# Optimization experiments

Hardware: AMD Instinct MI355X
Metric: run time of the kernel (lower is better)

## Reference

```python
import jax, jax.numpy as jnp
import numpy as np

# Static config matching init_kwargs / input_specs
B, C, H, W, T = 2, 128, 32, 32, 32
OUT = 256
WS, SHIFT, HEADS = 4, 2, 8
MLP = 4 * C
N = WS ** 3          # tokens per 4x4x4 window = 64
D_BLOCKS = 4         # depth=2 -> 2 (no-shift, shift) pairs


def _rel_idx():
    coords = np.stack(np.meshgrid(np.arange(WS), np.arange(WS), np.arange(WS), indexing='ij')).reshape(3, -1)
    rel = (coords[:, :, None] - coords[:, None, :]).transpose(1, 2, 0) + (WS - 1)
    return (rel[..., 0] * (2 * WS - 1) ** 2 + rel[..., 1] * (2 * WS - 1) + rel[..., 2]).astype(np.int32)

REL_IDX = jnp.asarray(_rel_idx())  # [N, N]


def _attn_mask():
    # Faithful port of Block.createmask (H,W,T already multiples of WS)
    img = np.zeros((H, W, T))
    sl = (slice(0, -WS), slice(-WS, -SHIFT), slice(-SHIFT, None))
    cnt = 0
    for hs in sl:
        for ws_ in sl:
            for ts in sl:
                img[hs, ws_, ts] = cnt
                cnt += 1
    m = img.reshape(H // WS, WS, W // WS, WS, T // WS, WS).transpose(0, 2, 4, 1, 3, 5).reshape(-1, N)
    am = m[:, None, :] - m[:, :, None]
    return jnp.asarray(np.where(am != 0, -100.0, 0.0).astype(np.float32))  # [nW, N, N]

MASK = _attn_mask()


def _partition(x):  # [b,H,W,T,c] -> [b*nW, N, c]
    b, c = x.shape[0], x.shape[-1]
    x = x.reshape(b, H // WS, WS, W // WS, WS, T // WS, WS, c).transpose(0, 1, 3, 5, 2, 4, 6, 7)
    return x.reshape(-1, N, c)


def _reverse(wins, b, c):  # [b*nW, N, c] -> [b,H,W,T,c]
    x = wins.reshape(b, H // WS, W // WS, T // WS, WS, WS, WS, c).transpose(0, 1, 4, 2, 5, 3, 6, 7)
    return x.reshape(b, H, W, T, c)


def _ln(x, g, b):
    mu = x.mean(-1, keepdims=True)
    var = ((x - mu) ** 2).mean(-1, keepdims=True)
    return (x - mu) / jnp.sqrt(var + 1e-5) * g + b


def _swin(x, shift, g1, b1, qw, qb, pw, pb, rpb, g2, b2, f1w, f1b, f2w, f2b):
    b, L, c = x.shape
    hd = c // HEADS
    scale = hd ** -0.5
    h = _ln(x, g1, b1).reshape(b, H, W, T, c)
    if shift:
        h = jnp.roll(h, (-SHIFT, -SHIFT, -SHIFT), axis=(1, 2, 3))
    win = _partition(h)  # [b*nW, N, c]
    qkv = (win @ qw.T + qb).reshape(-1, N, 3, HEADS, hd).transpose(2, 0, 3, 1, 4)
    q, k, v = qkv[0] * scale, qkv[1], qkv[2]
    attn = jnp.einsum('bhnd,bhmd->bhnm', q, k) + rpb[REL_IDX].transpose(2, 0, 1)[None]
    if shift:
        nW = MASK.shape[0]
        attn = (attn.reshape(b, nW, HEADS, N, N) + MASK[None, :, None]).reshape(-1, HEADS, N, N)
    attn = jax.nn.softmax(attn, axis=-1)
    o = jnp.einsum('bhnm,bhmd->bhnd', attn, v).transpose(0, 2, 1, 3).reshape(-1, N, c)
    o = o @ pw.T + pb
    h = _reverse(o, b, c)
    if shift:
        h = jnp.roll(h, (SHIFT, SHIFT, SHIFT), axis=(1, 2, 3))
    x = x + h.reshape(b, L, c)
    m = jax.nn.gelu(_ln(x, g2, b2) @ f1w.T + f1b, approximate=False)
    return x + (m @ f2w.T + f2b)


def setup_inputs() -> dict:
    key = jax.random.key(0)
    ks = jax.random.split(key, 10)
    r = lambda i, sh, s=0.02: jax.random.normal(ks[i], sh, jnp.float32) * s
    Dn = D_BLOCKS
    return {
        'x': jax.random.normal(ks[0], (B, C, H, W, T), jnp.float32),
        'norm1_g': jnp.ones((Dn, C), jnp.float32), 'norm1_b': jnp.zeros((Dn, C), jnp.float32),
        'qkv_w': r(1, (Dn, 3 * C, C)), 'qkv_b': jnp.zeros((Dn, 3 * C), jnp.float32),
        'proj_w': r(2, (Dn, C, C)), 'proj_b': jnp.zeros((Dn, C), jnp.float32),
        'rpb': r(3, (Dn, (2 * WS - 1) ** 3, HEADS)),
        'norm2_g': jnp.ones((Dn, C), jnp.float32), 'norm2_b': jnp.zeros((Dn, C), jnp.float32),
        'fc1_w': r(4, (Dn, MLP, C)), 'fc1_b': jnp.zeros((Dn, MLP), jnp.float32),
        'fc2_w': r(5, (Dn, C, MLP)), 'fc2_b': jnp.zeros((Dn, C), jnp.float32),
        'dw_w': r(6, (C, 1, 3, 3, 3), 0.1), 'dw_b': jnp.zeros((C,), jnp.float32),
        'pw_w': r(7, (OUT, C, 1, 1, 1), 0.05), 'pw_b': jnp.zeros((OUT,), jnp.float32),
        'bn_g': jnp.ones((OUT,), jnp.float32), 'bn_b': jnp.zeros((OUT,), jnp.float32),
    }


def reference(x, norm1_g, norm1_b, qkv_w, qkv_b, proj_w, proj_b, rpb, norm2_g, norm2_b,
              fc1_w, fc1_b, fc2_w, fc2_b, dw_w, dw_b, pw_w, pw_b, bn_g, bn_b):
    b = x.shape[0]
    t = x.transpose(0, 2, 3, 4, 1).reshape(b, H * W * T, C)  # b (h w t) c
    shifts = [0, SHIFT, 0, SHIFT]
    for i, s in enumerate(shifts):
        t = _swin(t, s, norm1_g[i], norm1_b[i], qkv_w[i], qkv_b[i], proj_w[i], proj_b[i],
                  rpb[i], norm2_g[i], norm2_b[i], fc1_w[i], fc1_b[i], fc2_w[i], fc2_b[i])
    y = t.reshape(b, H, W, T, C).transpose(0, 4, 1, 2, 3)
    # connectBlock: depthwise 3x3x3 conv + pointwise 1x1x1 conv + BatchNorm3d + ReLU
    dn = ('NCDHW', 'OIDHW', 'NCDHW')
    y = jax.lax.conv_general_dilated(y, dw_w, (1, 1, 1), 'SAME', dimension_numbers=dn,
                                     feature_group_count=C) + dw_b[None, :, None, None, None]
    y = jax.lax.conv_general_dilated(y, pw_w, (1, 1, 1), 'SAME', dimension_numbers=dn) + pw_b[None, :, None, None, None]
    mu = y.mean((0, 2, 3, 4), keepdims=True)
    var = ((y - mu) ** 2).mean((0, 2, 3, 4), keepdims=True)
    y = (y - mu) / jnp.sqrt(var + 1e-5) * bn_g[None, :, None, None, None] + bn_b[None, :, None, None, None]
    return jax.nn.relu(y)
```

## Files before the change

kernel.cpp:

```cpp
#include <hip/hip_runtime.h>
#include <hip/hip_bf16.h>
#include <cstddef>
#include <cstdint>

typedef __attribute__((ext_vector_type(8))) short short8;
typedef __attribute__((ext_vector_type(4))) short short4v;
typedef __attribute__((ext_vector_type(4))) float floatx4;
typedef __hip_bfloat16 bf16;

#define HEADS 8
#define TOK   65536
#define OUTC  256

__device__ inline float b2f(short s) {
    union { unsigned u; float f; } x;
    x.u = ((unsigned)(unsigned short)s) << 16;
    return x.f;
}

__device__ inline floatx4 mfma16(short4v a, short4v b, floatx4 c) {
#if __has_builtin(__builtin_amdgcn_mfma_f32_16x16x16bf16_1k)
    return __builtin_amdgcn_mfma_f32_16x16x16bf16_1k(a, b, c, 0, 0, 0);
#else
    floatx4 d;
    asm volatile("v_mfma_f32_16x16x16_bf16 %0, %1, %2, %3\n\ts_nop 7"
                 : "=v"(d) : "v"(a), "v"(b), "v"(c));
    return d;
#endif
}

__global__ __launch_bounds__(256) void transpose_in_kernel(
    const float* __restrict__ x, float* __restrict__ out)
{
    __shared__ float tile[128 * 65];
    int chunk = blockIdx.x;
    int tid = threadIdx.x;
    int b = chunk >> 9;
    int sp0 = (chunk & 511) * 64;
    #pragma unroll
    for (int l = 0; l < 32; ++l) {
        int idx = l * 256 + tid;
        int c = idx >> 6;
        int s = idx & 63;
        tile[c * 65 + s] = x[(((size_t)(b * 128 + c)) << 15) + sp0 + s];
    }
    __syncthreads();
    #pragma unroll
    for (int l = 0; l < 32; ++l) {
        int idx = l * 256 + tid;
        int s = idx >> 7;
        int c = idx & 127;
        out[((size_t)((b << 15) + sp0 + s)) * 128 + c] = tile[c * 65 + s];
    }
}

__global__ __launch_bounds__(256) void prep_kernel(
    const float* __restrict__ qkv_w, const float* __restrict__ proj_w,
    const float* __restrict__ fc1_w, const float* __restrict__ fc2_w,
    const float* __restrict__ pw_w, const float* __restrict__ dw_w,
    bf16* __restrict__ wbf, float* __restrict__ dwt, float* __restrict__ stats)
{
    int i = blockIdx.x * 256 + threadIdx.x;
    float v;
    if (i < 196608)       v = qkv_w[i];
    else if (i < 262144)  v = proj_w[i - 196608];
    else if (i < 524288)  v = fc1_w[i - 262144];
    else if (i < 786432)  v = fc2_w[i - 524288];
    else                  v = pw_w[i - 786432];
    wbf[i] = __float2bfloat16(v);
    if (i < 3456) {
        int c = i / 27, k = i % 27;
        dwt[k * 128 + c] = dw_w[i];
    }
    if (i < 512) stats[i] = 0.f;
}

__global__ __launch_bounds__(256) void pack_kernel(
    const float* __restrict__ fc1_w, const float* __restrict__ fc2_w,
    const float* __restrict__ rpb,
    bf16* __restrict__ pw1, bf16* __restrict__ pw2, float* __restrict__ rpbt)
{
    int t = blockIdx.x * 256 + threadIdx.x;
    int i = t >> 17;
    int rem = t & 131071;
    int type = rem >> 16;
    int idx = rem & 65535;
    int j = idx & 7, lane = (idx >> 3) & 63;
    int ln15 = lane & 15, quad = lane >> 4;
    if (type == 0) {
        int nt = (idx >> 9) & 1, kk = (idx >> 10) & 3, wv = (idx >> 12) & 3, cc = (idx >> 14) & 3;
        int row = cc * 128 + wv * 32 + nt * 16 + ln15;
        int col = kk * 32 + quad * 8 + j;
        pw1[i * 65536 + idx] = __float2bfloat16(fc1_w[(size_t)i * 65536 + row * 128 + col]);
    } else {
        int nt = (idx >> 9) & 1, ks = (idx >> 10) & 3, cc = (idx >> 12) & 3, wv = (idx >> 14) & 3;
        int row = wv * 32 + nt * 16 + ln15;
        int col = cc * 128 + ks * 32 + quad * 8 + j;
        pw2[i * 65536 + idx] = __float2bfloat16(fc2_w[(size_t)i * 65536 + row * 512 + col]);
    }
    if (t < 10976) {
        int li = t / 2744, r = t - li * 2744;
        int head = r / 343, jj = r - head * 343;
        rpbt[t] = rpb[li * 2744 + jj * 8 + head];
    }
}

__global__ __launch_bounds__(256) void rpe_expand_kernel(
    const float* __restrict__ rpb, float* __restrict__ rpe, int layer)
{
    int t = blockIdx.x * 256 + threadIdx.x;
    int j = t & 63, i = (t >> 6) & 63, head = (t >> 12) & 7, wt = t >> 15;
    int ih = i >> 4, iw = (i >> 2) & 3, it = i & 3;
    int jh = j >> 4, jw = (j >> 2) & 3, jt = j & 3;
    int ridx = ((ih - jh + 3) * 7 + (iw - jw + 3)) * 7 + (it - jt + 3);
    float v = rpb[layer * 2744 + ridx * 8 + head];
    if (wt) {
        bool ok = true;
        if (wt & 4) ok = ok && ((ih >= 2) == (jh >= 2));
        if (wt & 2) ok = ok && ((iw >= 2) == (jw >= 2));
        if (wt & 1) ok = ok && ((it >= 2) == (jt >= 2));
        if (!ok) v -= 100.f;
    }
    rpe[t] = v;
}

__global__ __launch_bounds__(256) void ln_window_kernel(
    const float* __restrict__ x, bf16* __restrict__ out,
    const float* __restrict__ g, const float* __restrict__ bta, int shift)
{
    int m = blockIdx.x * 4 + (threadIdx.x >> 6);
    int lane = threadIdx.x & 63;
    int n = m & 63, w = (m >> 6) & 511, b = m >> 15;
    int ih = n >> 4, iw = (n >> 2) & 3, it = n & 3;
    int wh = w >> 6, ww = (w >> 3) & 7, wt = w & 7;
    int h  = (wh * 4 + ih + shift) & 31;
    int w2 = (ww * 4 + iw + shift) & 31;
    int t  = (wt * 4 + it + shift) & 31;
    size_t tok = ((size_t)b << 15) + ((h * 32 + w2) * 32 + t);
    const float* xp = x + tok * 128;
    float v0 = xp[lane], v1 = xp[lane + 64];
    float s = v0 + v1, sq = v0 * v0 + v1 * v1;
    #pragma unroll
    for (int o = 32; o > 0; o >>= 1) { s += __shfl_xor(s, o); sq += __shfl_xor(sq, o); }
    float mu  = s * (1.0f / 128.0f);
    float var = sq * (1.0f / 128.0f) - mu * mu;
    float rs  = rsqrtf(var + 1e-5f);
    bf16* op = out + (size_t)m * 128;
    op[lane]      = __float2bfloat16((v0 - mu) * rs * g[lane]      + bta[lane]);
    op[lane + 64] = __float2bfloat16((v1 - mu) * rs * g[lane + 64] + bta[lane + 64]);
}

__global__ __launch_bounds__(256) void gemm_bf16_kernel(
    const bf16* __restrict__ A, const bf16* __restrict__ Bw,
    const float* __restrict__ bias, bf16* __restrict__ Cb, float* __restrict__ Cf,
    float* __restrict__ aux, const float* __restrict__ p1, const float* __restrict__ p2,
    int M, int N, int K, int mode, int shift)
{
    __shared__ __align__(16) char smem[34816];
    __shared__ float cs[128];
    __shared__ float cq[128];
    short* As = (short*)smem;
    short* Bs = (short*)(smem + 8192);
    int tid = threadIdx.x;
    int lane = tid & 63, wv = tid >> 6;
    int wm = wv >> 1, wn = wv & 1;
    int ln15 = lane & 15, quad = lane >> 4;
    int q8 = quad * 8;
    int nBase = blockIdx.x * 128;
    int mBase = blockIdx.y * 128;
    floatx4 acc[4][4] = {};

    if (mode == 4 && tid < 128) { cs[tid] = 0.f; cq[tid] = 0.f; }

    int srow = tid >> 2, scb = tid & 3;
    for (int k0 = 0; k0 < K; k0 += 32) {
        #pragma unroll
        for (int i = 0; i < 2; ++i) {
            int row = srow + i * 64;
            ((uint4*)As)[i * 256 + tid] =
                *(const uint4*)(A + (size_t)(mBase + row) * K + k0 + scb * 8);
            ((uint4*)Bs)[i * 256 + tid] =
                *(const uint4*)(Bw + (size_t)(nBase + row) * K + k0 + scb * 8);
        }
        __syncthreads();
        short8 af[4], bfr[4];
        #pragma unroll
        for (int mt = 0; mt < 4; ++mt)
            af[mt] = *(const short8*)&As[(wm * 64 + mt * 16 + ln15) * 32 + q8];
        #pragma unroll
        for (int nt = 0; nt < 4; ++nt)
            bfr[nt] = *(const short8*)&Bs[(wn * 64 + nt * 16 + ln15) * 32 + q8];
        #pragma unroll
        for (int mt = 0; mt < 4; ++mt)
            #pragma unroll
            for (int nt = 0; nt < 4; ++nt)
                acc[mt][nt] = __builtin_amdgcn_mfma_f32_16x16x32_bf16(
                    af[mt], bfr[nt], acc[mt][nt], 0, 0, 0);
        __syncthreads();
    }

    if (mode == 4) {
        #pragma unroll
        for (int nt = 0; nt < 4; ++nt) {
            int nl = wn * 64 + nt * 16 + ln15;
            float bs = bias[nBase + nl];
            float s = 0.f, sq = 0.f;
            #pragma unroll
            for (int mt = 0; mt < 4; ++mt)
                #pragma unroll
                for (int r = 0; r < 4; ++r) {
                    float v = acc[mt][nt][r] + bs;
                    s += v; sq += v * v;
                }
            atomicAdd(&cs[nl], s);
            atomicAdd(&cq[nl], sq);
        }
        __syncthreads();
        if (tid < 128) {
            atomicAdd(&aux[nBase + tid], cs[tid]);
            atomicAdd(&aux[256 + nBase + tid], cq[tid]);
        }
        return;
    }

    if (mode == 0) {
        bf16* estage = (bf16*)smem;
        float qsc = (shift && nBase == 0) ? 0.25f : 1.0f;
        #pragma unroll
        for (int mt = 0; mt < 4; ++mt)
            #pragma unroll
            for (int nt = 0; nt < 4; ++nt)
                #pragma unroll
                for (int r = 0; r < 4; ++r) {
                    int row = wm * 64 + mt * 16 + quad * 4 + r;
                    int col = wn * 64 + nt * 16 + ln15;
                    estage[row * 136 + col] =
                        __float2bfloat16((acc[mt][nt][r] + bias[nBase + col]) * qsc);
                }
        __syncthreads();
        int row = tid >> 1, hf = tid & 1;
        #pragma unroll
        for (int j = 0; j < 4; ++j) {
            int col = hf * 64 + j * 16;
            *(uint4*)(Cb + (size_t)(mBase + row) * N + nBase + col) =
                *(const uint4*)&estage[row * 136 + col];
            *(uint4*)(Cb + (size_t)(mBase + row) * N + nBase + col + 8) =
                *(const uint4*)&estage[row * 136 + col + 8];
        }
        return;
    }

    if (mode == 2) {
        float* fstage = (float*)smem;
        #pragma unroll
        for (int hf = 0; hf < 2; ++hf) {
            if (wm == hf) {
                #pragma unroll
                for (int mt = 0; mt < 4; ++mt)
                    #pragma unroll
                    for (int nt = 0; nt < 4; ++nt)
                        #pragma unroll
                        for (int r = 0; r < 4; ++r) {
                            int ml = mt * 16 + quad * 4 + r;
                            int col = wn * 64 + nt * 16 + ln15;
                            fstage[ml * 132 + col] = acc[mt][nt][r] + bias[col];
                        }
            }
            __syncthreads();
            int tl = tid >> 2, part = tid & 3;
            int g = mBase + hf * 64 + tl;
            int n_ = g & 63, w = (g >> 6) & 511, b = g >> 15;
            int ih = n_ >> 4, iw = (n_ >> 2) & 3, it = n_ & 3;
            int wh = w >> 6, ww = (w >> 3) & 7, wt = w & 7;
            int h  = (wh * 4 + ih + shift) & 31;
            int w2 = (ww * 4 + iw + shift) & 31;
            int t  = (wt * 4 + it + shift) & 31;
            size_t tok = ((size_t)b << 15) + ((h * 32 + w2) * 32 + t);
            float* dst = aux + tok * 128 + part * 32;
            #pragma unroll
            for (int j = 0; j < 8; ++j) {
                float4 a = *(float4*)(dst + j * 4);
                float4 l = *(const float4*)&fstage[tl * 132 + part * 32 + j * 4];
                a.x += l.x; a.y += l.y; a.z += l.z; a.w += l.w;
                *(float4*)(dst + j * 4) = a;
            }
            __syncthreads();
        }
        return;
    }

    {
        float* fstage = (float*)smem;
        int b = mBase >> 15, sp0 = mBase & 32767;
        #pragma unroll
        for (int hf = 0; hf < 2; ++hf) {
            if (wn == hf) {
                #pragma unroll
                for (int nt = 0; nt < 4; ++nt) {
                    int ncol = nt * 16 + ln15;
                    int nn = nBase + hf * 64 + ncol;
                    float mean = aux[nn] * (1.0f / 65536.0f);
                    float var  = aux[256 + nn] * (1.0f / 65536.0f) - mean * mean;
                    float sc = rsqrtf(var + 1e-5f) * p1[nn];
                    float off = p2[nn] + bias[nn] * sc - mean * sc;
                    #pragma unroll
                    for (int mt = 0; mt < 4; ++mt)
                        #pragma unroll
                        for (int r = 0; r < 4; ++r) {
                            int ml = wm * 64 + mt * 16 + quad * 4 + r;
                            float y = acc[mt][nt][r] * sc + off;
                            fstage[ncol * 132 + ml] = fmaxf(y, 0.f);
                        }
                }
            }
            __syncthreads();
            int nl = tid >> 2, part = tid & 3;
            int nn = nBase + hf * 64 + nl;
            float* dst = Cf + (((size_t)(b * 256 + nn)) << 15) + sp0 + part * 32;
            #pragma unroll
            for (int j = 0; j < 8; ++j)
                *(float4*)(dst + j * 4) = *(const float4*)&fstage[nl * 132 + part * 32 + j * 4];
            __syncthreads();
        }
    }
}

__global__ __launch_bounds__(256, 4) void mlp_kernel(
    float* __restrict__ xbuf, const float* __restrict__ g, const float* __restrict__ bta,
    const bf16* __restrict__ pw1, const float* __restrict__ b1,
    const bf16* __restrict__ pw2, const float* __restrict__ b2,
    bf16* __restrict__ xout16)
{
    __shared__ __align__(16) bf16 smem[64 * 136 * 2];
    bf16* aln  = smem;
    bf16* hidc = smem + 64 * 136;
    float* ostage = (float*)smem;
    int tid = threadIdx.x;
    int lane = tid & 63, wv = tid >> 6;
    int ln15 = lane & 15, quad = lane >> 4;
    int q8 = quad * 8;
    size_t tok0 = (size_t)blockIdx.x * 64;

    #pragma unroll
    for (int itk = 0; itk < 16; ++itk) {
        int t = wv * 16 + itk;
        const float* xp = xbuf + (tok0 + t) * 128;
        float v0 = xp[lane], v1 = xp[lane + 64];
        float s = v0 + v1, sq = v0 * v0 + v1 * v1;
        #pragma unroll
        for (int o = 32; o > 0; o >>= 1) { s += __shfl_xor(s, o); sq += __shfl_xor(sq, o); }
        float mu  = s * (1.0f / 128.0f);
        float var = sq * (1.0f / 128.0f) - mu * mu;
        float rs  = rsqrtf(var + 1e-5f);
        aln[t * 136 + lane]      = __float2bfloat16((v0 - mu) * rs * g[lane]      + bta[lane]);
        aln[t * 136 + lane + 64] = __float2bfloat16((v1 - mu) * rs * g[lane + 64] + bta[lane + 64]);
    }
    __syncthreads();

    floatx4 acc2[4][2] = {};
    #pragma unroll
    for (int cc = 0; cc < 4; ++cc) {
        floatx4 acc[4][2] = {};
        const bf16* p1w = pw1 + (size_t)(cc * 4 + wv) * 4096;
        #pragma unroll
        for (int kk = 0; kk < 4; ++kk) {
            short8 af[4], bfr[2];
            #pragma unroll
            for (int mt = 0; mt < 4; ++mt)
                af[mt] = *(const short8*)&aln[(mt * 16 + ln15) * 136 + kk * 32 + q8];
            #pragma unroll
            for (int nt = 0; nt < 2; ++nt)
                bfr[nt] = *(const short8*)(p1w + kk * 1024 + nt * 512 + lane * 8);
            #pragma unroll
            for (int mt = 0; mt < 4; ++mt)
                #pragma unroll
                for (int nt = 0; nt < 2; ++nt)
                    acc[mt][nt] = __builtin_amdgcn_mfma_f32_16x16x32_bf16(
                        af[mt], bfr[nt], acc[mt][nt], 0, 0, 0);
        }
        if (cc) __syncthreads();
        #pragma unroll
        for (int mt = 0; mt < 4; ++mt)
            #pragma unroll
            for (int nt = 0; nt < 2; ++nt)
                #pragma unroll
                for (int r = 0; r < 4; ++r) {
                    int m = mt * 16 + quad * 4 + r;
                    int ncl = wv * 32 + nt * 16 + ln15;
                    float v = acc[mt][nt][r] + b1[cc * 128 + ncl];
                    float u = v * (0.7978845608f + 0.0356774081f * v * v);
                    v = v * __builtin_amdgcn_rcpf(1.f + __expf(-2.f * u));
                    hidc[m * 136 + ncl] = __float2bfloat16(v);
                }
        __syncthreads();
        const bf16* p2w = pw2 + (size_t)(wv * 4 + cc) * 4096;
        #pragma unroll
        for (int ks = 0; ks < 4; ++ks) {
            short8 af[4], bfr[2];
            #pragma unroll
            for (int mt = 0; mt < 4; ++mt)
                af[mt] = *(const short8*)&hidc[(mt * 16 + ln15) * 136 + ks * 32 + q8];
            #pragma unroll
            for (int nt = 0; nt < 2; ++nt)
                bfr[nt] = *(const short8*)(p2w + ks * 1024 + nt * 512 + lane * 8);
            #pragma unroll
            for (int mt = 0; mt < 4; ++mt)
                #pragma unroll
                for (int nt = 0; nt < 2; ++nt)
                    acc2[mt][nt] = __builtin_amdgcn_mfma_f32_16x16x32_bf16(
                        af[mt], bfr[nt], acc2[mt][nt], 0, 0, 0);
        }
    }
    __syncthreads();

    #pragma unroll
    for (int mt = 0; mt < 4; ++mt)
        #pragma unroll
        for (int nt = 0; nt < 2; ++nt)
            #pragma unroll
            for (int r = 0; r < 4; ++r) {
                int m = mt * 16 + quad * 4 + r;
                int n = wv * 32 + nt * 16 + ln15;
                ostage[m * 132 + n] = acc2[mt][nt][r] + b2[n];
            }
    __syncthreads();

    #pragma unroll
    for (int jj = 0; jj < 8; ++jj) {
        int idx = (jj * 256 + tid) * 4;
        int t = idx >> 7, c = idx & 127;
        float4 v = *(const float4*)(xbuf + tok0 * 128 + idx);
        float4 o = *(const float4*)&ostage[t * 132 + c];
        v.x += o.x; v.y += o.y; v.z += o.z; v.w += o.w;
        *(float4*)(xbuf + tok0 * 128 + idx) = v;
        if (xout16) {
            __align__(8) bf16 hh[4];
            hh[0] = __float2bfloat16(v.x); hh[1] = __float2bfloat16(v.y);
            hh[2] = __float2bfloat16(v.z); hh[3] = __float2bfloat16(v.w);
            *(uint2*)(xout16 + tok0 * 128 + idx) = *(const uint2*)hh;
        }
    }
}

__global__ __launch_bounds__(256, 3) void attn_mfma_kernel(
    const bf16* __restrict__ qkv, const float* __restrict__ rpe,
    bf16* __restrict__ outp, int shift)
{
    __shared__ __align__(16) short qs[64 * 392];
    int tid = threadIdx.x;
    int lane = tid & 63, wv = tid >> 6;
    int ln15 = lane & 15, quad = lane >> 4;
    int win = blockIdx.x;
    size_t tok0 = (size_t)win * 64;

    const short* gq = (const short*)qkv + tok0 * 384;
    #pragma unroll
    for (int l = 0; l < 12; ++l) {
        int idx = l * 256 + tid;
        int r = idx / 48, c = idx - r * 48;
        *(uint4*)&qs[r * 392 + c * 8] = *(const uint4*)&gq[r * 384 + c * 8];
    }
    int w = win & 511;
    int wtype = 0;
    if (shift)
        wtype = (((w >> 6) == 7) << 2) | ((((w >> 3) & 7) == 7) << 1) | (int)((w & 7) == 7);
    const float* rpw = rpe + ((size_t)(wtype * 8) << 12);
    __syncthreads();

    floatx4 oacc[2][4];
    #pragma unroll
    for (int hh = 0; hh < 2; ++hh) {
        int head = wv * 2 + hh;
        const float* rph = rpw + ((size_t)head << 12);

        floatx4 acc[4][4];
        #pragma unroll
        for (int jt = 0; jt < 4; ++jt)
            #pragma unroll
            for (int it = 0; it < 4; ++it)
                acc[jt][it] = *(const floatx4*)&rph[(it * 16 + ln15) * 64 + jt * 16 + quad * 4];

        short4v qf[4], kf[4];
        #pragma unroll
        for (int it = 0; it < 4; ++it)
            qf[it] = *(const short4v*)&qs[(it * 16 + ln15) * 392 + head * 16 + quad * 4];
        #pragma unroll
        for (int jt = 0; jt < 4; ++jt)
            kf[jt] = *(const short4v*)&qs[(jt * 16 + ln15) * 392 + 128 + head * 16 + quad * 4];

        #pragma unroll
        for (int jt = 0; jt < 4; ++jt)
            #pragma unroll
            for (int it = 0; it < 4; ++it)
                acc[jt][it] = mfma16(kf[jt], qf[it], acc[jt][it]);

        short4v pf[4][4];
        #pragma unroll
        for (int it = 0; it < 4; ++it) {
            float m = -1e30f;
            #pragma unroll
            for (int jt = 0; jt < 4; ++jt)
                #pragma unroll
                for (int r = 0; r < 4; ++r) m = fmaxf(m, acc[jt][it][r]);
            m = fmaxf(m, __shfl_xor(m, 16));
            m = fmaxf(m, __shfl_xor(m, 32));
            float s = 0.f;
            #pragma unroll
            for (int jt = 0; jt < 4; ++jt)
                #pragma unroll
                for (int r = 0; r < 4; ++r) {
                    float e = __expf(acc[jt][it][r] - m);
                    acc[jt][it][r] = e; s += e;
                }
            s += __shfl_xor(s, 16);
            s += __shfl_xor(s, 32);
            float inv = 1.0f / s;
            #pragma unroll
            for (int jt = 0; jt < 4; ++jt) {
                __align__(8) bf16 pb[4];
                #pragma unroll
                for (int r = 0; r < 4; ++r)
                    pb[r] = __float2bfloat16(acc[jt][it][r] * inv);
                pf[jt][it] = *(const short4v*)pb;
            }
        }

        short4v vf[4];
        #pragma unroll
        for (int jt = 0; jt < 4; ++jt)
            #pragma unroll
            for (int jj = 0; jj < 4; ++jj)
                vf[jt][jj] = qs[(jt * 16 + quad * 4 + jj) * 392 + 256 + head * 16 + ln15];

        #pragma unroll
        for (int it = 0; it < 4; ++it) {
            floatx4 o = {0.f, 0.f, 0.f, 0.f};
            #pragma unroll
            for (int jt = 0; jt < 4; ++jt)
                o = mfma16(vf[jt], pf[jt][it], o);
            oacc[hh][it] = o;
        }
    }
    __syncthreads();

    short* ob = qs;
    #pragma unroll
    for (int hh = 0; hh < 2; ++hh)
        #pragma unroll
        for (int it = 0; it < 4; ++it) {
            __align__(8) bf16 t4[4];
            #pragma unroll
            for (int r = 0; r < 4; ++r) t4[r] = __float2bfloat16(oacc[hh][it][r]);
            *(short4v*)&ob[(it * 16 + ln15) * 136 + (wv * 2 + hh) * 16 + quad * 4] =
                *(const short4v*)t4;
        }
    __syncthreads();

    short* po = (short*)outp + tok0 * 128;
    #pragma unroll
    for (int l = 0; l < 4; ++l) {
        int idx = l * 256 + tid;
        int r = idx >> 4, c = idx & 15;
        *(uint4*)&po[r * 128 + c * 8] = *(const uint4*)&ob[r * 136 + c * 8];
    }
}

__global__ __launch_bounds__(256) void dwconv_kernel(
    const bf16* __restrict__ x, const float* __restrict__ dwt,
    const float* __restrict__ bias, bf16* __restrict__ out)
{
    int blk = blockIdx.x;
    int b = blk >> 9;
    int h = (blk >> 4) & 31;
    int w = ((blk & 15) << 1) | (threadIdx.x >> 7);
    int tid = threadIdx.x & 127;
    int c0 = (tid & 31) * 4;
    int t0 = (tid >> 5) * 8;

    float4 acc[8];
    float4 bs = *(const float4*)&bias[c0];
    #pragma unroll
    for (int o = 0; o < 8; ++o) acc[o] = bs;

    #pragma unroll
    for (int kh = 0; kh < 3; ++kh) {
        int hh = h + kh - 1;
        if (hh < 0 || hh > 31) continue;
        #pragma unroll
        for (int kw = 0; kw < 3; ++kw) {
            int ww = w + kw - 1;
            if (ww < 0 || ww > 31) continue;
            const short* px = (const short*)x +
                ((size_t)(b << 15) + (hh * 32 + ww) * 32) * 128 + c0;
            float4 v[10];
            #pragma unroll
            for (int u = 0; u < 10; ++u) {
                int tt = t0 - 1 + u;
                if (tt >= 0 && tt < 32) {
                    short4v s4 = *(const short4v*)(px + (size_t)tt * 128);
                    v[u].x = b2f(s4[0]); v[u].y = b2f(s4[1]);
                    v[u].z = b2f(s4[2]); v[u].w = b2f(s4[3]);
                } else {
                    v[u].x = v[u].y = v[u].z = v[u].w = 0.f;
                }
            }
            int kb = kh * 9 + kw * 3;
            float4 w0 = *(const float4*)&dwt[(kb + 0) * 128 + c0];
            float4 w1 = *(const float4*)&dwt[(kb + 1) * 128 + c0];
            float4 w2 = *(const float4*)&dwt[(kb + 2) * 128 + c0];
            #pragma unroll
            for (int o = 0; o < 8; ++o) {
                acc[o].x += v[o].x * w0.x + v[o + 1].x * w1.x + v[o + 2].x * w2.x;
                acc[o].y += v[o].y * w0.y + v[o + 1].y * w1.y + v[o + 2].y * w2.y;
                acc[o].z += v[o].z * w0.z + v[o + 1].z * w1.z + v[o + 2].z * w2.z;
                acc[o].w += v[o].w * w0.w + v[o + 1].w * w1.w + v[o + 2].w * w2.w;
            }
        }
    }
    short* po = (short*)out + ((size_t)(b << 15) + (h * 32 + w) * 32 + t0) * 128 + c0;
    #pragma unroll
    for (int o = 0; o < 8; ++o) {
        __align__(8) bf16 h4[4];
        h4[0] = __float2bfloat16(acc[o].x);
        h4[1] = __float2bfloat16(acc[o].y);
        h4[2] = __float2bfloat16(acc[o].z);
        h4[3] = __float2bfloat16(acc[o].w);
        *(uint2*)(po + (size_t)o * 128) = *(const uint2*)h4;
    }
}

extern "C" void kernel_launch(void* const* d_in, const int* in_sizes, int n_in,
                              void* d_out, int out_size, void* d_ws, size_t ws_size,
                              hipStream_t stream)
{
    const float* x_in    = (const float*)d_in[0];
    const float* norm1_g = (const float*)d_in[1];
    const float* norm1_b = (const float*)d_in[2];
    const float* qkv_w   = (const float*)d_in[3];
    const float* qkv_b   = (const float*)d_in[4];
    const float* proj_w  = (const float*)d_in[5];
    const float* proj_b  = (const float*)d_in[6];
    const float* rpb     = (const float*)d_in[7];
    const float* norm2_g = (const float*)d_in[8];
    const float* norm2_b = (const float*)d_in[9];
    const float* fc1_w   = (const float*)d_in[10];
    const float* fc1_b   = (const float*)d_in[11];
    const float* fc2_w   = (const float*)d_in[12];
    const float* fc2_b   = (const float*)d_in[13];
    const float* dw_w    = (const float*)d_in[14];
    const float* dw_b    = (const float*)d_in[15];
    const float* pw_w    = (const float*)d_in[16];
    const float* pw_b    = (const float*)d_in[17];
    const float* bn_g    = (const float*)d_in[18];
    const float* bn_b    = (const float*)d_in[19];
    float* out = (float*)d_out;

    char* ws = (char*)d_ws;
    float* xbuf   = (float*)ws;
    bf16*  wbf    = (bf16*)(ws + 33554432ULL);
    float* dwt    = (float*)(ws + 35651584ULL);
    float* stats  = (float*)(ws + 35717120ULL);
    bf16*  pw1    = (bf16*)(ws + 35782656ULL);
    bf16*  pw2    = (bf16*)(ws + 36306944ULL);
    float* rpbt   = (float*)(ws + 36831232ULL);
    bf16*  lnbuf  = (bf16*)(ws + 37748736ULL);
    bf16*  attnbuf= (bf16*)(ws + 54525952ULL);
    bf16*  qkvbuf = (bf16*)(ws + 71303168ULL);
    bf16*  dwbuf  = attnbuf;
    bf16*  dcbuf  = lnbuf;
    float* rpe    = (float*)lnbuf;

    bf16* wqkv  = wbf;
    bf16* wproj = wbf + 196608;
    bf16* wpw   = wbf + 786432;

    hipLaunchKernelGGL(prep_kernel, dim3(3200), dim3(256), 0, stream,
                       qkv_w, proj_w, fc1_w, fc2_w, pw_w, dw_w, wbf, dwt, stats);
    hipLaunchKernelGGL(pack_kernel, dim3(2048), dim3(256), 0, stream,
                       fc1_w, fc2_w, rpb, pw1, pw2, rpbt);
    hipLaunchKernelGGL(transpose_in_kernel, dim3(1024), dim3(256), 0, stream, x_in, xbuf);

    const int shifts[4] = {0, 2, 0, 2};
    for (int i = 0; i < 4; ++i) {
        int s = shifts[i];
        hipLaunchKernelGGL(ln_window_kernel, dim3(TOK / 4), dim3(256), 0, stream,
                           xbuf, lnbuf, norm1_g + i * 128, norm1_b + i * 128, s);
        hipLaunchKernelGGL(gemm_bf16_kernel, dim3(3, TOK / 128), dim3(256), 0, stream,
                           lnbuf, wqkv + (size_t)i * 49152, qkv_b + i * 384,
                           qkvbuf, (float*)nullptr, (float*)nullptr,
                           (const float*)nullptr, (const float*)nullptr,
                           TOK, 384, 128, 0, 1 );
        hipLaunchKernelGGL(rpe_expand_kernel, dim3(s ? 1024 : 128), dim3(256), 0, stream,
                           rpb, rpe, i);
        hipLaunchKernelGGL(attn_mfma_kernel, dim3(TOK / 64), dim3(256), 0, stream,
                           qkvbuf, rpe, attnbuf, s);
        hipLaunchKernelGGL(gemm_bf16_kernel, dim3(1, TOK / 128), dim3(256), 0, stream,
                           attnbuf, wproj + (size_t)i * 16384, proj_b + i * 128,
                           (bf16*)nullptr, (float*)nullptr, xbuf,
                           (const float*)nullptr, (const float*)nullptr,
                           TOK, 128, 128, 2, s);
        hipLaunchKernelGGL(mlp_kernel, dim3(TOK / 64), dim3(256), 0, stream,
                           xbuf, norm2_g + i * 128, norm2_b + i * 128,
                           pw1 + (size_t)i * 65536, fc1_b + i * 512,
                           pw2 + (size_t)i * 65536, fc2_b + i * 128,
                           (i == 3) ? dwbuf : (bf16*)nullptr);
    }

    hipLaunchKernelGGL(dwconv_kernel, dim3(1024), dim3(256), 0, stream,
                       dwbuf, dwt, dw_b, dcbuf);
    hipLaunchKernelGGL(gemm_bf16_kernel, dim3(OUTC / 128, TOK / 128), dim3(256), 0, stream,
                       dcbuf, wpw, pw_b,
                       (bf16*)nullptr, (float*)nullptr, stats,
                       (const float*)nullptr, (const float*)nullptr,
                       TOK, OUTC, 128, 4, 0);
    hipLaunchKernelGGL(gemm_bf16_kernel, dim3(OUTC / 128, TOK / 128), dim3(256), 0, stream,
                       dcbuf, wpw, pw_b,
                       (bf16*)nullptr, out, stats,
                       bn_g, bn_b,
                       TOK, OUTC, 128, 5, 0);
}
```

Before: 744.4 us.

## Fuse LayerNorm-1 and window gather into QKV GEMM using precomputed token stats

Removes the standalone ln_window kernel. Per-token mean and rstd are now computed by the producers: the input transpose kernel for the first layer and the MLP epilogue for later layers. The QKV GEMM then gathers the shifted-window rows straight from the fp32 residual buffer, normalizes them and converts to bf16 while staging A tiles. This avoids a full bf16 write and read of the normalized activations plus one launch per layer. In exchange the A loads become fp32 gathers with extra ALU in the GEMM mainloop. The q-scale condition was also changed to apply on both shift settings.

```diff
diff --git a/kernel.cpp b/kernel.cpp
--- a/kernel.cpp
+++ b/kernel.cpp
@@ -30,7 +30,7 @@
 }
 
 __global__ __launch_bounds__(256) void transpose_in_kernel(
-    const float* __restrict__ x, float* __restrict__ out)
+    const float* __restrict__ x, float* __restrict__ out, float* __restrict__ tstats)
 {
     __shared__ float tile[128 * 65];
     int chunk = blockIdx.x;
@@ -51,6 +51,22 @@
         int s = idx >> 7;
         int c = idx & 127;
         out[((size_t)((b << 15) + sp0 + s)) * 128 + c] = tile[c * 65 + s];
+    }
+    int s = tid >> 2, q = tid & 3;
+    float sm = 0.f, sq = 0.f;
+    #pragma unroll
+    for (int cc = 0; cc < 32; ++cc) {
+        float v = tile[(q * 32 + cc) * 65 + s];
+        sm += v; sq += v * v;
+    }
+    sm += __shfl_xor(sm, 1); sq += __shfl_xor(sq, 1);
+    sm += __shfl_xor(sm, 2); sq += __shfl_xor(sq, 2);
+    if (q == 0) {
+        float mu = sm * (1.0f / 128.0f);
+        float var = sq * (1.0f / 128.0f) - mu * mu;
+        size_t tok = (size_t)(b << 15) + sp0 + s;
+        tstats[tok * 2]     = mu;
+        tstats[tok * 2 + 1] = rsqrtf(var + 1e-5f);
     }
 }
 
@@ -77,8 +93,7 @@
 
 __global__ __launch_bounds__(256) void pack_kernel(
     const float* __restrict__ fc1_w, const float* __restrict__ fc2_w,
-    const float* __restrict__ rpb,
-    bf16* __restrict__ pw1, bf16* __restrict__ pw2, float* __restrict__ rpbt)
+    bf16* __restrict__ pw1, bf16* __restrict__ pw2)
 {
     int t = blockIdx.x * 256 + threadIdx.x;
     int i = t >> 17;
@@ -98,11 +113,6 @@
         int col = cc * 128 + ks * 32 + quad * 8 + j;
         pw2[i * 65536 + idx] = __float2bfloat16(fc2_w[(size_t)i * 65536 + row * 512 + col]);
     }
-    if (t < 10976) {
-        int li = t / 2744, r = t - li * 2744;
-        int head = r / 343, jj = r - head * 343;
-        rpbt[t] = rpb[li * 2744 + jj * 8 + head];
-    }
 }
 
 __global__ __launch_bounds__(256) void rpe_expand_kernel(
@@ -122,32 +132,6 @@
         if (!ok) v -= 100.f;
     }
     rpe[t] = v;
-}
-
-__global__ __launch_bounds__(256) void ln_window_kernel(
-    const float* __restrict__ x, bf16* __restrict__ out,
-    const float* __restrict__ g, const float* __restrict__ bta, int shift)
-{
-    int m = blockIdx.x * 4 + (threadIdx.x >> 6);
-    int lane = threadIdx.x & 63;
-    int n = m & 63, w = (m >> 6) & 511, b = m >> 15;
-    int ih = n >> 4, iw = (n >> 2) & 3, it = n & 3;
-    int wh = w >> 6, ww = (w >> 3) & 7, wt = w & 7;
-    int h  = (wh * 4 + ih + shift) & 31;
-    int w2 = (ww * 4 + iw + shift) & 31;
-    int t  = (wt * 4 + it + shift) & 31;
-    size_t tok = ((size_t)b << 15) + ((h * 32 + w2) * 32 + t);
-    const float* xp = x + tok * 128;
-    float v0 = xp[lane], v1 = xp[lane + 64];
-    float s = v0 + v1, sq = v0 * v0 + v1 * v1;
-    #pragma unroll
-    for (int o = 32; o > 0; o >>= 1) { s += __shfl_xor(s, o); sq += __shfl_xor(sq, o); }
-    float mu  = s * (1.0f / 128.0f);
-    float var = sq * (1.0f / 128.0f) - mu * mu;
-    float rs  = rsqrtf(var + 1e-5f);
-    bf16* op = out + (size_t)m * 128;
-    op[lane]      = __float2bfloat16((v0 - mu) * rs * g[lane]      + bta[lane]);
-    op[lane + 64] = __float2bfloat16((v1 - mu) * rs * g[lane + 64] + bta[lane + 64]);
 }
 
 __global__ __launch_bounds__(256) void gemm_bf16_kernel(
@@ -173,14 +157,57 @@
     if (mode == 4 && tid < 128) { cs[tid] = 0.f; cq[tid] = 0.f; }
 
     int srow = tid >> 2, scb = tid & 3;
+
+    int toks[2]; float tmu[2], trs[2];
+    if (mode == 0) {
+        if (tid < 128) { cs[tid] = p1[tid]; cq[tid] = p2[tid]; }
+        #pragma unroll
+        for (int i = 0; i < 2; ++i) {
+            int m = mBase + srow + i * 64;
+            int n = m & 63, w = (m >> 6) & 511, b = m >> 15;
+            int ih = n >> 4, iw = (n >> 2) & 3, it = n & 3;
+            int wh = w >> 6, ww = (w >> 3) & 7, wt = w & 7;
+            int h  = (wh * 4 + ih + shift) & 31;
+            int w2 = (ww * 4 + iw + shift) & 31;
+            int t  = (wt * 4 + it + shift) & 31;
+            toks[i] = (b << 15) + ((h * 32 + w2) * 32 + t);
+            tmu[i] = aux[(size_t)toks[i] * 2];
+            trs[i] = aux[(size_t)toks[i] * 2 + 1];
+        }
+        __syncthreads();
+    }
+
     for (int k0 = 0; k0 < K; k0 += 32) {
-        #pragma unroll
-        for (int i = 0; i < 2; ++i) {
-            int row = srow + i * 64;
-            ((uint4*)As)[i * 256 + tid] =
-                *(const uint4*)(A + (size_t)(mBase + row) * K + k0 + scb * 8);
-            ((uint4*)Bs)[i * 256 + tid] =
-                *(const uint4*)(Bw + (size_t)(nBase + row) * K + k0 + scb * 8);
+        if (mode == 0) {
+            int cb = k0 + scb * 8;
+            #pragma unroll
+            for (int i = 0; i < 2; ++i) {
+                const float* xr = Cf + (size_t)toks[i] * 128 + cb;
+                float4 a0 = *(const float4*)xr;
+                float4 a1 = *(const float4*)(xr + 4);
+                float mu = tmu[i], rs = trs[i];
+                __align__(16) bf16 pk[8];
+                pk[0] = __float2bfloat16((a0.x - mu) * rs * cs[cb + 0] + cq[cb + 0]);
+                pk[1] = __float2bfloat16((a0.y - mu) * rs * cs[cb + 1] + cq[cb + 1]);
+                pk[2] = __float2bfloat16((a0.z - mu) * rs * cs[cb + 2] + cq[cb + 2]);
+                pk[3] = __float2bfloat16((a0.w - mu) * rs * cs[cb + 3] + cq[cb + 3]);
+                pk[4] = __float2bfloat16((a1.x - mu) * rs * cs[cb + 4] + cq[cb + 4]);
+                pk[5] = __float2bfloat16((a1.y - mu) * rs * cs[cb + 5] + cq[cb + 5]);
+                pk[6] = __float2bfloat16((a1.z - mu) * rs * cs[cb + 6] + cq[cb + 6]);
+                pk[7] = __float2bfloat16((a1.w - mu) * rs * cs[cb + 7] + cq[cb + 7]);
+                ((uint4*)As)[i * 256 + tid] = *(const uint4*)pk;
+                ((uint4*)Bs)[i * 256 + tid] =
+                    *(const uint4*)(Bw + (size_t)(nBase + srow + i * 64) * K + cb);
+            }
+        } else {
+            #pragma unroll
+            for (int i = 0; i < 2; ++i) {
+                int row = srow + i * 64;
+                ((uint4*)As)[i * 256 + tid] =
+                    *(const uint4*)(A + (size_t)(mBase + row) * K + k0 + scb * 8);
+                ((uint4*)Bs)[i * 256 + tid] =
+                    *(const uint4*)(Bw + (size_t)(nBase + row) * K + k0 + scb * 8);
+            }
         }
         __syncthreads();
         short8 af[4], bfr[4];
@@ -225,7 +252,7 @@
 
     if (mode == 0) {
         bf16* estage = (bf16*)smem;
-        float qsc = (shift && nBase == 0) ? 0.25f : 1.0f;
+        float qsc = (nBase == 0) ? 0.25f : 1.0f;
         #pragma unroll
         for (int mt = 0; mt < 4; ++mt)
             #pragma unroll
@@ -329,7 +356,7 @@
     float* __restrict__ xbuf, const float* __restrict__ g, const float* __restrict__ bta,
     const bf16* __restrict__ pw1, const float* __restrict__ b1,
     const bf16* __restrict__ pw2, const float* __restrict__ b2,
-    bf16* __restrict__ xout16)
+    bf16* __restrict__ xout16, float* __restrict__ tstats)
 {
     __shared__ __align__(16) bf16 smem[64 * 136 * 2];
     bf16* aln  = smem;
@@ -438,6 +465,19 @@
             hh[0] = __float2bfloat16(v.x); hh[1] = __float2bfloat16(v.y);
             hh[2] = __float2bfloat16(v.z); hh[3] = __float2bfloat16(v.w);
             *(uint2*)(xout16 + tok0 * 128 + idx) = *(const uint2*)hh;
+        }
+        float ps = v.x + v.y + v.z + v.w;
+        float pq = v.x * v.x + v.y * v.y + v.z * v.z + v.w * v.w;
+        #pragma unroll
+        for (int o2 = 16; o2 > 0; o2 >>= 1) {
+            ps += __shfl_xor(ps, o2); pq += __shfl_xor(pq, o2);
+        }
+        if ((tid & 31) == 0) {
+            float mu = ps * (1.0f / 128.0f);
+            float var = pq * (1.0f / 128.0f) - mu * mu;
+            size_t tok = tok0 + t;
+            tstats[tok * 2]     = mu;
+            tstats[tok * 2 + 1] = rsqrtf(var + 1e-5f);
         }
     }
 }
@@ -662,7 +702,7 @@
     float* stats  = (float*)(ws + 35717120ULL);
     bf16*  pw1    = (bf16*)(ws + 35782656ULL);
     bf16*  pw2    = (bf16*)(ws + 36306944ULL);
-    float* rpbt   = (float*)(ws + 36831232ULL);
+    float* tstats = (float*)(ws + 36831232ULL);
     bf16*  lnbuf  = (bf16*)(ws + 37748736ULL);
     bf16*  attnbuf= (bf16*)(ws + 54525952ULL);
     bf16*  qkvbuf = (bf16*)(ws + 71303168ULL);
@@ -677,19 +717,18 @@
     hipLaunchKernelGGL(prep_kernel, dim3(3200), dim3(256), 0, stream,
                        qkv_w, proj_w, fc1_w, fc2_w, pw_w, dw_w, wbf, dwt, stats);
     hipLaunchKernelGGL(pack_kernel, dim3(2048), dim3(256), 0, stream,
-                       fc1_w, fc2_w, rpb, pw1, pw2, rpbt);
-    hipLaunchKernelGGL(transpose_in_kernel, dim3(1024), dim3(256), 0, stream, x_in, xbuf);
+                       fc1_w, fc2_w, pw1, pw2);
+    hipLaunchKernelGGL(transpose_in_kernel, dim3(1024), dim3(256), 0, stream,
+                       x_in, xbuf, tstats);
 
     const int shifts[4] = {0, 2, 0, 2};
     for (int i = 0; i < 4; ++i) {
         int s = shifts[i];
-        hipLaunchKernelGGL(ln_window_kernel, dim3(TOK / 4), dim3(256), 0, stream,
-                           xbuf, lnbuf, norm1_g + i * 128, norm1_b + i * 128, s);
         hipLaunchKernelGGL(gemm_bf16_kernel, dim3(3, TOK / 128), dim3(256), 0, stream,
-                           lnbuf, wqkv + (size_t)i * 49152, qkv_b + i * 384,
-                           qkvbuf, (float*)nullptr, (float*)nullptr,
-                           (const float*)nullptr, (const float*)nullptr,
-                           TOK, 384, 128, 0, 1 );
+                           (const bf16*)nullptr, wqkv + (size_t)i * 49152, qkv_b + i * 384,
+                           qkvbuf, xbuf, tstats,
+                           norm1_g + i * 128, norm1_b + i * 128,
+                           TOK, 384, 128, 0, s);
         hipLaunchKernelGGL(rpe_expand_kernel, dim3(s ? 1024 : 128), dim3(256), 0, stream,
                            rpb, rpe, i);
         hipLaunchKernelGGL(attn_mfma_kernel, dim3(TOK / 64), dim3(256), 0, stream,
@@ -703,7 +742,7 @@
                            xbuf, norm2_g + i * 128, norm2_b + i * 128,
                            pw1 + (size_t)i * 65536, fc1_b + i * 512,
                            pw2 + (size_t)i * 65536, fc2_b + i * 128,
-                           (i == 3) ? dwbuf : (bf16*)nullptr);
+                           (i == 3) ? dwbuf : (bf16*)nullptr, tstats);
     }
 
     hipLaunchKernelGGL(dwconv_kernel, dim3(1024), dim3(256), 0, stream,
```

Result: no change. 757.9 us (+1.8%).
